# Kernel tuning notes

Hardware: AMD Instinct MI355X
Metric: run time of the kernel (lower is better)

## Reference

```python
import jax, jax.numpy as jnp
import numpy as np

N_USERS = 100000
N_MOVIES = 50000
EMB_DIM = 64
N_EDGES = 5000000


def setup_inputs() -> dict:
    key = jax.random.key(0)
    k1, k2, k3 = jax.random.split(key, 3)
    N = N_USERS + N_MOVIES
    edge_index = jax.random.randint(k1, (2, N_EDGES), 0, N, dtype=jnp.int64)
    user_emb = 0.1 * jax.random.normal(k2, (N_USERS, EMB_DIM), dtype=jnp.float32)
    movie_emb = 0.1 * jax.random.normal(k3, (N_MOVIES, EMB_DIM), dtype=jnp.float32)
    return {"edge_index": edge_index, "n_layers": 3,
            "user_emb": user_emb, "movie_emb": movie_emb}


def reference(edge_index, n_layers, user_emb, movie_emb):
    n_users = user_emb.shape[0]
    N = n_users + movie_emb.shape[0]
    x = jnp.concatenate([user_emb, movie_emb], axis=0)  # [N, D]

    row, col = edge_index[0], edge_index[1]  # source -> target
    # gcn_norm without self-loops (LGConv default): deg from target (col)
    deg = jnp.zeros((N,), x.dtype).at[col].add(1.0)
    dis = jnp.where(deg > 0, jax.lax.rsqrt(jnp.maximum(deg, 1.0)), 0.0)
    norm = dis[row] * dis[col]  # [E]

    acc = x
    total = x
    for _ in range(n_layers):
        msg = acc[row] * norm[:, None]            # [E, D] gather + scale
        acc = jax.ops.segment_sum(msg, col, num_segments=N)  # scatter-add
        total = total + acc
    final = total / (n_layers + 1)                # mean over layers 0..K
    return final[:n_users], final[n_users:]
```

## Files before the change

### kernel.cpp

```cpp
#include <hip/hip_runtime.h>

typedef _Float16 half_t;
typedef _Float16 half2_t __attribute__((ext_vector_type(2)));
union pk_u { unsigned int u; half2_t h; };

#define EMB 64
#define NLAYERS 3
#define BSH2 9
#define BW2 512
#define NB2MAX 512
#define CAP 20480
#define EGCAP 28672
#define P1_BATCH 4096
#define P1_TH 512
#define P1_EPT 8
#define BINTH 1024

__device__ inline void scan_512w(const int* __restrict__ in, int* __restrict__ lstart,
                                 int* __restrict__ pair) {
    int t = threadIdx.x;
    int a0 = 0, a1 = 0;
    if (t < 256) { a0 = in[2 * t]; a1 = in[2 * t + 1]; pair[t] = a0 + a1; }
    __syncthreads();
    for (int off = 1; off < 256; off <<= 1) {
        int u = 0;
        if (t < 256 && t >= off) u = pair[t - off];
        __syncthreads();
        if (t < 256) pair[t] += u;
        __syncthreads();
    }
    if (t < 256) {
        lstart[2 * t]     = pair[t] - a0 - a1;
        lstart[2 * t + 1] = pair[t] - a1;
    }
    __syncthreads();
}

__global__ __launch_bounds__(512) void part_kernel(
        const int* __restrict__ row, const int* __restrict__ col,
        int* __restrict__ gcount, int* __restrict__ tmp, int E, int nb2) {
    __shared__ int hist[NB2MAX];
    __shared__ int lstart[NB2MAX];
    __shared__ int gbase[NB2MAX];
    __shared__ int pair[256];
    __shared__ int srec[P1_BATCH];
    __shared__ unsigned short sbuck[P1_BATCH];

    int base = blockIdx.x * P1_BATCH;
    int nE = min(P1_BATCH, E - base);

    for (int i = threadIdx.x; i < NB2MAX; i += P1_TH) hist[i] = 0;
    __syncthreads();

    int myc[P1_EPT];
    #pragma unroll
    for (int k = 0; k < P1_EPT; ++k) {
        int idx = base + (k << 9) + threadIdx.x;
        int c = (idx < E) ? col[idx] : -1;
        myc[k] = c;
        if (c >= 0) atomicAdd(&hist[c >> BSH2], 1);
    }
    __syncthreads();

    scan_512w(hist, lstart, pair);

    for (int b = threadIdx.x; b < nb2; b += P1_TH) {
        int c = hist[b];
        int off = 0;
        if (c > 0) off = atomicAdd(&gcount[b], c);
        gbase[b] = b * CAP + off - lstart[b];
    }
    __syncthreads();
    for (int b = threadIdx.x; b < NB2MAX; b += P1_TH) hist[b] = lstart[b];
    __syncthreads();

    #pragma unroll
    for (int k = 0; k < P1_EPT; ++k) {
        int idx = base + (k << 9) + threadIdx.x;
        if (idx < E) {
            int c = myc[k];
            int b = c >> BSH2;
            int r = row[idx];
            int pos = atomicAdd(&hist[b], 1);
            srec[pos] = (r << BSH2) | (c & (BW2 - 1));
            sbuck[pos] = (unsigned short)b;
        }
    }
    __syncthreads();

    for (int i = threadIdx.x; i < nE; i += P1_TH)
        tmp[gbase[sbuck[i]] + i] = srec[i];
}

__global__ __launch_bounds__(1024) void bin_kernel(
        const int* __restrict__ tmp, const int* __restrict__ gcount,
        int* __restrict__ eg, int2* __restrict__ sd, float* __restrict__ dis,
        const float4* __restrict__ uev, const float4* __restrict__ mev,
        float4* __restrict__ outv, uint2* __restrict__ s0v,
        int n_users, int N) {
    __shared__ int hist[BW2];
    __shared__ int padh[BW2];
    __shared__ int lstart[BW2];
    __shared__ int pair[256];
    __shared__ float sdis[BW2];
    int b = blockIdx.x;
    int cnt = gcount[b];
    int rbase = b * CAP;
    int ebase = b * EGCAP;
    int c0 = b << BSH2;
    int nc = min(BW2, N - c0);
    int sent = N << 4;

    for (int i = threadIdx.x; i < BW2; i += BINTH) hist[i] = 0;
    __syncthreads();
    for (int i = threadIdx.x; i < cnt; i += BINTH)
        atomicAdd(&hist[tmp[rbase + i] & (BW2 - 1)], 1);
    __syncthreads();

    for (int c = threadIdx.x; c < BW2; c += BINTH)
        padh[c] = (hist[c] + 31) & ~31;
    __syncthreads();

    scan_512w(padh, lstart, pair);

    for (int c = threadIdx.x; c < nc; c += BINTH) {
        int d = hist[c];
        float dn = (d > 0) ? rsqrtf((float)d) : 0.0f;
        sd[c0 + c] = make_int2(ebase + lstart[c], padh[c]);
        dis[c0 + c] = dn;
        sdis[c] = dn;
    }
    __syncthreads();
    for (int i = threadIdx.x; i < BW2; i += BINTH) hist[i] = lstart[i];
    __syncthreads();

    for (int i = threadIdx.x; i < cnt; i += BINTH) {
        int v = tmp[rbase + i];
        int pos = atomicAdd(&hist[v & (BW2 - 1)], 1);
        eg[ebase + pos] = (v >> BSH2) << 4;
    }
    __syncthreads();

    for (int i = threadIdx.x; i < BW2 * 32; i += BINTH) {
        int c = i >> 5;
        int o = i & 31;
        int st = hist[c];
        int en = lstart[c] + padh[c];
        if (st + o < en) eg[ebase + st + o] = sent;
    }
    int tot = lstart[BW2 - 1] + padh[BW2 - 1];
    if (threadIdx.x < 64) eg[ebase + tot + threadIdx.x] = sent;

    for (int i = threadIdx.x; i < nc * 16; i += BINTH) {
        int loc = i >> 4;
        int node = c0 + loc;
        int q = i & 15;
        const float4* src = (node < n_users) ? (uev + (long long)node * 16)
                                             : (mev + (long long)(node - n_users) * 16);
        float4 v = src[q];
        outv[(long long)node * 16 + q] = v;
        float dn = sdis[loc];
        pk_u w0, w1;
        w0.h[0] = (half_t)(v.x * dn); w0.h[1] = (half_t)(v.y * dn);
        w1.h[0] = (half_t)(v.z * dn); w1.h[1] = (half_t)(v.w * dn);
        s0v[(long long)node * 16 + q] = make_uint2(w0.u, w1.u);
    }
}

template <bool LAST>
__global__ __launch_bounds__(256) void gather_kernel(
        const int* __restrict__ eg, const int2* __restrict__ sd,
        const float* __restrict__ dis,
        const uint4* __restrict__ tab, uint2* __restrict__ sB,
        float4* __restrict__ outv, float scale, int N) {
    int wave = blockIdx.x * (blockDim.x >> 6) + (threadIdx.x >> 6);
    if (wave >= N) return;
    int l = threadIdx.x & 63;
    int p = l & 7;
    int h = l >> 3;
    unsigned pb = (unsigned)p << 4;
    const char* tb = (const char*)tab;

    int2 se = sd[wave];
    int j = se.x;
    int e = se.x + se.y;
    pk_u a0, a1, a2, a3;
    a0.u = 0; a1.u = 0; a2.u = 0; a3.u = 0;

    if (j < e) {
        int r0 = eg[j + h];
        int r1 = eg[j + 8 + h];
        int r2 = eg[j + 16 + h];
        int r3 = eg[j + 24 + h];
        for (; j < e; j += 32) {
            int n0 = eg[j + 32 + h];
            int n1 = eg[j + 40 + h];
            int n2 = eg[j + 48 + h];
            int n3 = eg[j + 56 + h];
            uint4 v0 = *(const uint4*)(tb + ((unsigned)(r0 << 3) + pb));
            uint4 v1 = *(const uint4*)(tb + ((unsigned)(r1 << 3) + pb));
            uint4 v2 = *(const uint4*)(tb + ((unsigned)(r2 << 3) + pb));
            uint4 v3 = *(const uint4*)(tb + ((unsigned)(r3 << 3) + pb));
            pk_u t;
            t.u = v0.x; a0.h += t.h; t.u = v0.y; a1.h += t.h;
            t.u = v0.z; a2.h += t.h; t.u = v0.w; a3.h += t.h;
            t.u = v1.x; a0.h += t.h; t.u = v1.y; a1.h += t.h;
            t.u = v1.z; a2.h += t.h; t.u = v1.w; a3.h += t.h;
            t.u = v2.x; a0.h += t.h; t.u = v2.y; a1.h += t.h;
            t.u = v2.z; a2.h += t.h; t.u = v2.w; a3.h += t.h;
            t.u = v3.x; a0.h += t.h; t.u = v3.y; a1.h += t.h;
            t.u = v3.z; a2.h += t.h; t.u = v3.w; a3.h += t.h;
            r0 = n0; r1 = n1; r2 = n2; r3 = n3;
        }
    }

    #pragma unroll
    for (int m = 8; m <= 32; m <<= 1) {
        pk_u t;
        t.u = (unsigned int)__shfl_xor((int)a0.u, m); a0.h += t.h;
        t.u = (unsigned int)__shfl_xor((int)a1.u, m); a1.h += t.h;
        t.u = (unsigned int)__shfl_xor((int)a2.u, m); a2.h += t.h;
        t.u = (unsigned int)__shfl_xor((int)a3.u, m); a3.h += t.h;
    }

    if (h < 2) {
        pk_u x0 = h ? a2 : a0;
        pk_u x1 = h ? a3 : a1;
        float dc = dis[wave];
        float g0 = dc * (float)x0.h[0];
        float g1 = dc * (float)x0.h[1];
        float g2 = dc * (float)x1.h[0];
        float g3 = dc * (float)x1.h[1];
        long long o = (long long)wave * 16 + p * 2 + h;
        float4 v = outv[o];
        v.x = (v.x + g0) * scale;
        v.y = (v.y + g1) * scale;
        v.z = (v.z + g2) * scale;
        v.w = (v.w + g3) * scale;
        outv[o] = v;
        if (!LAST) {
            pk_u w0, w1;
            w0.h[0] = (half_t)(dc * g0); w0.h[1] = (half_t)(dc * g1);
            w1.h[0] = (half_t)(dc * g2); w1.h[1] = (half_t)(dc * g3);
            sB[o] = make_uint2(w0.u, w1.u);
        }
    }
}

extern "C" void kernel_launch(void* const* d_in, const int* in_sizes, int n_in,
                              void* d_out, int out_size, void* d_ws, size_t ws_size,
                              hipStream_t stream) {
    const int*   edge = (const int*)d_in[0];
    const float* ue   = (const float*)d_in[2];
    const float* me   = (const float*)d_in[3];
    float*       out  = (float*)d_out;

    const int E        = in_sizes[0] / 2;
    const int n_users  = in_sizes[2] / EMB;
    const int n_movies = in_sizes[3] / EMB;
    const int N        = n_users + n_movies;
    const int* row = edge;
    const int* col = edge + E;
    const int nb2 = (N + BW2 - 1) >> BSH2;

    char* ws = (char*)d_ws;
    auto align_up = [](size_t v) { return (v + 255) & ~(size_t)255; };
    int*    gcount = (int*)ws;    ws += align_up((size_t)NB2MAX * sizeof(int));
    int2*   sd     = (int2*)ws;   ws += align_up((size_t)N * sizeof(int2));
    float*  dis    = (float*)ws;  ws += align_up((size_t)N * sizeof(float));
    int*    tmp    = (int*)ws;    ws += align_up((size_t)nb2 * CAP * sizeof(int));
    int*    eg     = (int*)ws;    ws += align_up((size_t)nb2 * EGCAP * sizeof(int));
    half_t* sA     = (half_t*)ws; ws += align_up((size_t)(N + 1) * EMB * sizeof(half_t));
    half_t* sB     = (half_t*)ws; ws += align_up((size_t)(N + 1) * EMB * sizeof(half_t));

    hipMemsetAsync(gcount, 0, (size_t)NB2MAX * sizeof(int), stream);
    hipMemsetAsync(sA + (size_t)N * EMB, 0, EMB * sizeof(half_t), stream);
    hipMemsetAsync(sB + (size_t)N * EMB, 0, EMB * sizeof(half_t), stream);
    part_kernel<<<(E + P1_BATCH - 1) / P1_BATCH, P1_TH, 0, stream>>>(
        row, col, gcount, tmp, E, nb2);
    bin_kernel<<<nb2, BINTH, 0, stream>>>(
        tmp, gcount, eg, sd, dis,
        (const float4*)ue, (const float4*)me, (float4*)out, (uint2*)sA,
        n_users, N);

    const int waves_per_block = 4;
    const int gblocks = (N + waves_per_block - 1) / waves_per_block;
    gather_kernel<false><<<gblocks, 256, 0, stream>>>(
        eg, sd, dis, (const uint4*)sA, (uint2*)sB, (float4*)out, 1.0f, N);
    gather_kernel<false><<<gblocks, 256, 0, stream>>>(
        eg, sd, dis, (const uint4*)sB, (uint2*)sA, (float4*)out, 1.0f, N);
    gather_kernel<true><<<gblocks, 256, 0, stream>>>(
        eg, sd, dis, (const uint4*)sA, (uint2*)sB, (float4*)out,
        1.0f / (NLAYERS + 1), N);
}
```

Measured before the change: 492.9 us.

## Defer fp32 output accumulation to final layer, store intermediate layers in half

Intermediate layer results are written as fp16 into reused scratch buffers (tmp and the output buffer), so the float output is no longer read-modified-written every layer. The last layer reads the inputs, both stored layers and its own result, and writes the mean once. Separately, the gather loop is widened to 64 edges per iteration with padding raised to 64 and row indices pre-shifted to byte offsets, and the global bucket counters are spread onto separate cache lines to reduce atomic contention. Intermediate layers are now kept in fp16 rather than fp32, which costs some precision, and low-degree nodes carry more padding edges.

```diff
diff --git a/kernel.cpp b/kernel.cpp
--- a/kernel.cpp
+++ b/kernel.cpp
@@ -9,8 +9,9 @@
 #define BSH2 9
 #define BW2 512
 #define NB2MAX 512
+#define GSPREAD 32
 #define CAP 20480
-#define EGCAP 28672
+#define EGCAP 34816
 #define P1_BATCH 4096
 #define P1_TH 512
 #define P1_EPT 8
@@ -67,7 +68,7 @@
     for (int b = threadIdx.x; b < nb2; b += P1_TH) {
         int c = hist[b];
         int off = 0;
-        if (c > 0) off = atomicAdd(&gcount[b], c);
+        if (c > 0) off = atomicAdd(&gcount[b * GSPREAD], c);
         gbase[b] = b * CAP + off - lstart[b];
     }
     __syncthreads();
@@ -96,7 +97,7 @@
         const int* __restrict__ tmp, const int* __restrict__ gcount,
         int* __restrict__ eg, int2* __restrict__ sd, float* __restrict__ dis,
         const float4* __restrict__ uev, const float4* __restrict__ mev,
-        float4* __restrict__ outv, uint2* __restrict__ s0v,
+        uint2* __restrict__ s0v,
         int n_users, int N) {
     __shared__ int hist[BW2];
     __shared__ int padh[BW2];
@@ -104,12 +105,12 @@
     __shared__ int pair[256];
     __shared__ float sdis[BW2];
     int b = blockIdx.x;
-    int cnt = gcount[b];
+    int cnt = gcount[b * GSPREAD];
     int rbase = b * CAP;
     int ebase = b * EGCAP;
     int c0 = b << BSH2;
     int nc = min(BW2, N - c0);
-    int sent = N << 4;
+    int sent = N << 7;
 
     for (int i = threadIdx.x; i < BW2; i += BINTH) hist[i] = 0;
     __syncthreads();
@@ -118,7 +119,7 @@
     __syncthreads();
 
     for (int c = threadIdx.x; c < BW2; c += BINTH)
-        padh[c] = (hist[c] + 31) & ~31;
+        padh[c] = (hist[c] + 63) & ~63;
     __syncthreads();
 
     scan_512w(padh, lstart, pair);
@@ -137,19 +138,14 @@
     for (int i = threadIdx.x; i < cnt; i += BINTH) {
         int v = tmp[rbase + i];
         int pos = atomicAdd(&hist[v & (BW2 - 1)], 1);
-        eg[ebase + pos] = (v >> BSH2) << 4;
-    }
-    __syncthreads();
-
-    for (int i = threadIdx.x; i < BW2 * 32; i += BINTH) {
-        int c = i >> 5;
-        int o = i & 31;
-        int st = hist[c];
+        eg[ebase + pos] = (v >> BSH2) << 7;
+    }
+    __syncthreads();
+
+    for (int c = threadIdx.x; c < nc; c += BINTH) {
         int en = lstart[c] + padh[c];
-        if (st + o < en) eg[ebase + st + o] = sent;
-    }
-    int tot = lstart[BW2 - 1] + padh[BW2 - 1];
-    if (threadIdx.x < 64) eg[ebase + tot + threadIdx.x] = sent;
+        for (int ppos = hist[c]; ppos < en; ++ppos) eg[ebase + ppos] = sent;
+    }
 
     for (int i = threadIdx.x; i < nc * 16; i += BINTH) {
         int loc = i >> 4;
@@ -158,7 +154,6 @@
         const float4* src = (node < n_users) ? (uev + (long long)node * 16)
                                              : (mev + (long long)(node - n_users) * 16);
         float4 v = src[q];
-        outv[(long long)node * 16 + q] = v;
         float dn = sdis[loc];
         pk_u w0, w1;
         w0.h[0] = (half_t)(v.x * dn); w0.h[1] = (half_t)(v.y * dn);
@@ -167,12 +162,15 @@
     }
 }
 
-template <bool LAST>
+template <int LAYER>
 __global__ __launch_bounds__(256) void gather_kernel(
         const int* __restrict__ eg, const int2* __restrict__ sd,
         const float* __restrict__ dis,
-        const uint4* __restrict__ tab, uint2* __restrict__ sB,
-        float4* __restrict__ outv, float scale, int N) {
+        const uint4* __restrict__ tab, uint2* __restrict__ sOut,
+        uint2* __restrict__ uOut,
+        const uint2* __restrict__ u1, const uint2* __restrict__ u2,
+        const float4* __restrict__ uev, const float4* __restrict__ mev,
+        float4* __restrict__ outv, int n_users, int N) {
     int wave = blockIdx.x * (blockDim.x >> 6) + (threadIdx.x >> 6);
     if (wave >= N) return;
     int l = threadIdx.x & 63;
@@ -187,31 +185,40 @@
     pk_u a0, a1, a2, a3;
     a0.u = 0; a1.u = 0; a2.u = 0; a3.u = 0;
 
-    if (j < e) {
+    for (; j < e; j += 64) {
         int r0 = eg[j + h];
         int r1 = eg[j + 8 + h];
         int r2 = eg[j + 16 + h];
         int r3 = eg[j + 24 + h];
-        for (; j < e; j += 32) {
-            int n0 = eg[j + 32 + h];
-            int n1 = eg[j + 40 + h];
-            int n2 = eg[j + 48 + h];
-            int n3 = eg[j + 56 + h];
-            uint4 v0 = *(const uint4*)(tb + ((unsigned)(r0 << 3) + pb));
-            uint4 v1 = *(const uint4*)(tb + ((unsigned)(r1 << 3) + pb));
-            uint4 v2 = *(const uint4*)(tb + ((unsigned)(r2 << 3) + pb));
-            uint4 v3 = *(const uint4*)(tb + ((unsigned)(r3 << 3) + pb));
-            pk_u t;
-            t.u = v0.x; a0.h += t.h; t.u = v0.y; a1.h += t.h;
-            t.u = v0.z; a2.h += t.h; t.u = v0.w; a3.h += t.h;
-            t.u = v1.x; a0.h += t.h; t.u = v1.y; a1.h += t.h;
-            t.u = v1.z; a2.h += t.h; t.u = v1.w; a3.h += t.h;
-            t.u = v2.x; a0.h += t.h; t.u = v2.y; a1.h += t.h;
-            t.u = v2.z; a2.h += t.h; t.u = v2.w; a3.h += t.h;
-            t.u = v3.x; a0.h += t.h; t.u = v3.y; a1.h += t.h;
-            t.u = v3.z; a2.h += t.h; t.u = v3.w; a3.h += t.h;
-            r0 = n0; r1 = n1; r2 = n2; r3 = n3;
-        }
+        int r4 = eg[j + 32 + h];
+        int r5 = eg[j + 40 + h];
+        int r6 = eg[j + 48 + h];
+        int r7 = eg[j + 56 + h];
+        uint4 v0 = *(const uint4*)(tb + ((unsigned)r0 + pb));
+        uint4 v1 = *(const uint4*)(tb + ((unsigned)r1 + pb));
+        uint4 v2 = *(const uint4*)(tb + ((unsigned)r2 + pb));
+        uint4 v3 = *(const uint4*)(tb + ((unsigned)r3 + pb));
+        uint4 v4 = *(const uint4*)(tb + ((unsigned)r4 + pb));
+        uint4 v5 = *(const uint4*)(tb + ((unsigned)r5 + pb));
+        uint4 v6 = *(const uint4*)(tb + ((unsigned)r6 + pb));
+        uint4 v7 = *(const uint4*)(tb + ((unsigned)r7 + pb));
+        pk_u t;
+        t.u = v0.x; a0.h += t.h; t.u = v0.y; a1.h += t.h;
+        t.u = v0.z; a2.h += t.h; t.u = v0.w; a3.h += t.h;
+        t.u = v1.x; a0.h += t.h; t.u = v1.y; a1.h += t.h;
+        t.u = v1.z; a2.h += t.h; t.u = v1.w; a3.h += t.h;
+        t.u = v2.x; a0.h += t.h; t.u = v2.y; a1.h += t.h;
+        t.u = v2.z; a2.h += t.h; t.u = v2.w; a3.h += t.h;
+        t.u = v3.x; a0.h += t.h; t.u = v3.y; a1.h += t.h;
+        t.u = v3.z; a2.h += t.h; t.u = v3.w; a3.h += t.h;
+        t.u = v4.x; a0.h += t.h; t.u = v4.y; a1.h += t.h;
+        t.u = v4.z; a2.h += t.h; t.u = v4.w; a3.h += t.h;
+        t.u = v5.x; a0.h += t.h; t.u = v5.y; a1.h += t.h;
+        t.u = v5.z; a2.h += t.h; t.u = v5.w; a3.h += t.h;
+        t.u = v6.x; a0.h += t.h; t.u = v6.y; a1.h += t.h;
+        t.u = v6.z; a2.h += t.h; t.u = v6.w; a3.h += t.h;
+        t.u = v7.x; a0.h += t.h; t.u = v7.y; a1.h += t.h;
+        t.u = v7.z; a2.h += t.h; t.u = v7.w; a3.h += t.h;
     }
 
     #pragma unroll
@@ -231,18 +238,31 @@
         float g1 = dc * (float)x0.h[1];
         float g2 = dc * (float)x1.h[0];
         float g3 = dc * (float)x1.h[1];
-        long long o = (long long)wave * 16 + p * 2 + h;
-        float4 v = outv[o];
-        v.x = (v.x + g0) * scale;
-        v.y = (v.y + g1) * scale;
-        v.z = (v.z + g2) * scale;
-        v.w = (v.w + g3) * scale;
-        outv[o] = v;
-        if (!LAST) {
-            pk_u w0, w1;
+        int q = p * 2 + h;
+        long long o16 = (long long)wave * 16 + q;
+        if (LAYER < 3) {
+            pk_u w0, w1, uw0, uw1;
             w0.h[0] = (half_t)(dc * g0); w0.h[1] = (half_t)(dc * g1);
             w1.h[0] = (half_t)(dc * g2); w1.h[1] = (half_t)(dc * g3);
-            sB[o] = make_uint2(w0.u, w1.u);
+            uw0.h[0] = (half_t)g0; uw0.h[1] = (half_t)g1;
+            uw1.h[0] = (half_t)g2; uw1.h[1] = (half_t)g3;
+            sOut[o16] = make_uint2(w0.u, w1.u);
+            long long uo = (LAYER == 1) ? o16 : ((long long)wave * 32 + q);
+            uOut[uo] = make_uint2(uw0.u, uw1.u);
+        } else {
+            const float4* src = (wave < n_users) ? (uev + (long long)wave * 16)
+                                                 : (mev + (long long)(wave - n_users) * 16);
+            float4 xv = src[q];
+            uint2 ua2 = u1[o16];
+            uint2 ub2 = u2[(long long)wave * 32 + q];
+            pk_u pa, pb2, pc, pd;
+            pa.u = ua2.x; pb2.u = ua2.y; pc.u = ub2.x; pd.u = ub2.y;
+            float4 r;
+            r.x = (xv.x + (float)pa.h[0]  + (float)pc.h[0] + g0) * 0.25f;
+            r.y = (xv.y + (float)pa.h[1]  + (float)pc.h[1] + g1) * 0.25f;
+            r.z = (xv.z + (float)pb2.h[0] + (float)pd.h[0] + g2) * 0.25f;
+            r.w = (xv.w + (float)pb2.h[1] + (float)pd.h[1] + g3) * 0.25f;
+            outv[o16] = r;
         }
     }
 }
@@ -265,31 +285,36 @@
 
     char* ws = (char*)d_ws;
     auto align_up = [](size_t v) { return (v + 255) & ~(size_t)255; };
-    int*    gcount = (int*)ws;    ws += align_up((size_t)NB2MAX * sizeof(int));
+    int*    gcount = (int*)ws;    ws += align_up((size_t)NB2MAX * GSPREAD * sizeof(int));
     int2*   sd     = (int2*)ws;   ws += align_up((size_t)N * sizeof(int2));
     float*  dis    = (float*)ws;  ws += align_up((size_t)N * sizeof(float));
     int*    tmp    = (int*)ws;    ws += align_up((size_t)nb2 * CAP * sizeof(int));
     int*    eg     = (int*)ws;    ws += align_up((size_t)nb2 * EGCAP * sizeof(int));
     half_t* sA     = (half_t*)ws; ws += align_up((size_t)(N + 1) * EMB * sizeof(half_t));
     half_t* sB     = (half_t*)ws; ws += align_up((size_t)(N + 1) * EMB * sizeof(half_t));
-
-    hipMemsetAsync(gcount, 0, (size_t)NB2MAX * sizeof(int), stream);
+    uint2* u1 = (uint2*)tmp;
+    uint2* u2 = (uint2*)out;
+
+    hipMemsetAsync(gcount, 0, (size_t)NB2MAX * GSPREAD * sizeof(int), stream);
     hipMemsetAsync(sA + (size_t)N * EMB, 0, EMB * sizeof(half_t), stream);
     hipMemsetAsync(sB + (size_t)N * EMB, 0, EMB * sizeof(half_t), stream);
     part_kernel<<<(E + P1_BATCH - 1) / P1_BATCH, P1_TH, 0, stream>>>(
         row, col, gcount, tmp, E, nb2);
     bin_kernel<<<nb2, BINTH, 0, stream>>>(
         tmp, gcount, eg, sd, dis,
-        (const float4*)ue, (const float4*)me, (float4*)out, (uint2*)sA,
+        (const float4*)ue, (const float4*)me, (uint2*)sA,
         n_users, N);
 
     const int waves_per_block = 4;
     const int gblocks = (N + waves_per_block - 1) / waves_per_block;
-    gather_kernel<false><<<gblocks, 256, 0, stream>>>(
-        eg, sd, dis, (const uint4*)sA, (uint2*)sB, (float4*)out, 1.0f, N);
-    gather_kernel<false><<<gblocks, 256, 0, stream>>>(
-        eg, sd, dis, (const uint4*)sB, (uint2*)sA, (float4*)out, 1.0f, N);
-    gather_kernel<true><<<gblocks, 256, 0, stream>>>(
-        eg, sd, dis, (const uint4*)sA, (uint2*)sB, (float4*)out,
-        1.0f / (NLAYERS + 1), N);
-}
+    gather_kernel<1><<<gblocks, 256, 0, stream>>>(
+        eg, sd, dis, (const uint4*)sA, (uint2*)sB, u1,
+        nullptr, nullptr, nullptr, nullptr, nullptr, n_users, N);
+    gather_kernel<2><<<gblocks, 256, 0, stream>>>(
+        eg, sd, dis, (const uint4*)sB, (uint2*)sA, u2,
+        nullptr, nullptr, nullptr, nullptr, nullptr, n_users, N);
+    gather_kernel<3><<<gblocks, 256, 0, stream>>>(
+        eg, sd, dis, (const uint4*)sA, nullptr, nullptr,
+        (const uint2*)u1, (const uint2*)u2,
+        (const float4*)ue, (const float4*)me, (float4*)out, n_users, N);
+}
```

New measurement: 487.7 us. No clear change (-1.1%).
